# Performance work log

Hardware: AMD Instinct MI355X
Metric: run time of the kernel (lower is better)

Reference implementation:

```python
import math
import jax, jax.numpy as jnp
import numpy as np

B, C, T = 4, 512, 1024
H = 8
KC = C // H
WIN = 4


def _get_relative_embeddings(emb, length):
    win = (emb.shape[1] - 1) // 2
    pad_length = max(length - (win + 1), 0)
    slice_start = max(win + 1 - length, 0)
    slice_end = slice_start + 2 * length - 1
    if pad_length > 0:
        emb = jnp.pad(emb, ((0, 0), (pad_length, pad_length), (0, 0)))
    return emb[:, slice_start:slice_end]


def _relative_to_absolute(x):
    # x: [b, h, L, 2L-1] -> [b, h, L, L] via skew trick
    b, h, L, _ = x.shape
    x = jnp.pad(x, ((0, 0), (0, 0), (0, 0), (0, 1)))          # [b,h,L,2L]
    x_flat = x.reshape(b, h, L * 2 * L)
    x_flat = jnp.pad(x_flat, ((0, 0), (0, 0), (0, L - 1)))    # [b,h,(L+1)(2L-1)]
    x_final = x_flat.reshape(b, h, L + 1, 2 * L - 1)
    return x_final[:, :, :L, L - 1:]


def _absolute_to_relative(x):
    # x: [b, h, L, L] -> [b, h, L, 2L-1]
    b, h, L, _ = x.shape
    x = jnp.pad(x, ((0, 0), (0, 0), (0, 0), (0, L - 1)))      # [b,h,L,2L-1]
    x_flat = x.reshape(b, h, L * (2 * L - 1))
    x_flat = jnp.pad(x_flat, ((0, 0), (0, 0), (L, 0)))        # [b,h,2L^2]
    x_final = x_flat.reshape(b, h, L, 2 * L)
    return x_final[:, :, :, 1:]


def setup_inputs() -> dict:
    key = jax.random.key(0)
    ks = jax.random.split(key, 12)
    xavier = math.sqrt(6.0 / (C + C))  # xavier_uniform for [C, C, 1] conv weight
    rel_std = KC ** (-0.5)
    return {
        "x": jax.random.normal(ks[0], (B, C, T), dtype=jnp.float32),
        "wq": jax.random.uniform(ks[1], (C, C), jnp.float32, -xavier, xavier),
        "bq": jnp.zeros((C,), jnp.float32),
        "wk": jax.random.uniform(ks[2], (C, C), jnp.float32, -xavier, xavier),
        "bk": jnp.zeros((C,), jnp.float32),
        "wv": jax.random.uniform(ks[3], (C, C), jnp.float32, -xavier, xavier),
        "bv": jnp.zeros((C,), jnp.float32),
        "wo": jax.random.normal(ks[4], (C, C), jnp.float32) * (1.0 / math.sqrt(C)),
        "bo": jnp.zeros((C,), jnp.float32),
        "emb_rel_k": jax.random.normal(ks[5], (1, 2 * WIN + 1, KC), jnp.float32) * rel_std,
        "emb_rel_v": jax.random.normal(ks[6], (1, 2 * WIN + 1, KC), jnp.float32) * rel_std,
    }


def reference(x, wq, bq, wk, bk, wv, bv, wo, bo, emb_rel_k, emb_rel_v):
    b, c, t = x.shape
    # 1x1 conv == channel matmul
    q = jnp.einsum("oi,bit->bot", wq, x) + bq[:, None]
    k = jnp.einsum("oi,bit->bot", wk, x) + bk[:, None]
    v = jnp.einsum("oi,bit->bot", wv, x) + bv[:, None]
    # [b, H, t, kc]
    q = q.reshape(b, H, KC, t).transpose(0, 1, 3, 2)
    k = k.reshape(b, H, KC, t).transpose(0, 1, 3, 2)
    v = v.reshape(b, H, KC, t).transpose(0, 1, 3, 2)
    inv_sqrt = 1.0 / math.sqrt(KC)
    scores = jnp.einsum("bhtc,bhsc->bhts", q, k) * inv_sqrt
    rel_k = _get_relative_embeddings(emb_rel_k, t)[0]            # [2t-1, kc]
    rel_logits = jnp.einsum("bhtc,rc->bhtr", q, rel_k)           # [b,h,t,2t-1]
    scores = scores + _relative_to_absolute(rel_logits) * inv_sqrt
    p_attn = jax.nn.softmax(scores, axis=-1)
    output = jnp.einsum("bhts,bhsc->bhtc", p_attn, v)
    rel_weights = _absolute_to_relative(p_attn)                  # [b,h,t,2t-1]
    rel_v = _get_relative_embeddings(emb_rel_v, t)[0]            # [2t-1, kc]
    output = output + jnp.einsum("bhtr,rc->bhtc", rel_weights, rel_v)
    output = output.transpose(0, 1, 3, 2).reshape(b, c, t)
    return jnp.einsum("oi,bit->bot", wo, output) + bo[:, None]
```

## Files before the change

kernel.cpp:

```cpp
#include <hip/hip_runtime.h>
#include <hip/hip_bf16.h>

#define Bdim 4
#define Cdim 512
#define Tdim 1024
#define Hn   8
#define KCd  64

typedef __attribute__((ext_vector_type(8))) short bf16x8;
typedef __attribute__((ext_vector_type(4))) float f32x4;

__device__ __forceinline__ unsigned short f32_bf16_rne(float f) {
    unsigned u = __float_as_uint(f);
    u += 0x7FFFu + ((u >> 16) & 1u);
    return (unsigned short)(u >> 16);
}
__device__ __forceinline__ float bf16_f32(unsigned short h) {
    return __uint_as_float(((unsigned)h) << 16);
}

__device__ __forceinline__ int off_row(int row, int c) {
    return (((row >> 4) * 2 + (c >> 5)) << 9)
         + (((((c >> 3) & 3) << 4) + (row & 15)) << 3) + (c & 7);
}
__device__ __forceinline__ int off_col(int c, int j) {
    return (((c >> 4) * 2 + (j >> 5)) << 9)
         + (((((j >> 3) & 3) << 4) + (c & 15)) << 3) + (j & 7);
}

__device__ __forceinline__ int sw(int row, int col) {
    return (row << 6) + ((((col >> 3) ^ (row & 7)) << 3) | (col & 7));
}
__device__ __forceinline__ bf16x8 fragld(const unsigned short* a, int row, int kstep, int quad) {
    return *(const bf16x8*)&a[(row << 6) + ((((kstep << 2) | quad) ^ (row & 7)) << 3)];
}

#define BM 128
#define BN 64
#define BK 32
#define LDK 40

__global__ __launch_bounds__(256) void gemm3_mfma(
    int mode,
    const float* __restrict__ w0, const float* __restrict__ w1, const float* __restrict__ w2,
    const float* __restrict__ b0, const float* __restrict__ b1, const float* __restrict__ b2,
    const float* __restrict__ x,
    unsigned short* __restrict__ qhi, unsigned short* __restrict__ qlo,
    unsigned short* __restrict__ khi, unsigned short* __restrict__ klo,
    unsigned short* __restrict__ vhi, unsigned short* __restrict__ vlo,
    float* __restrict__ ofp)
{
    __shared__ unsigned short Whi[BM][LDK], Wlo[BM][LDK];
    __shared__ unsigned short Xhi[BN][LDK], Xlo[BN][LDK];

    const int tid = threadIdx.x;

    int bx, by, b;
    {
        const int n = blockIdx.x;
        const int xcd = n & 7, slot = n >> 3;
        if (mode == 0) {
            const int stripe = (xcd << 3) | (slot / 12);
            by = slot % 12;
            bx = stripe & 15;
            b  = stripe >> 4;
        } else {
            const int stripe = (xcd << 3) | (slot >> 2);
            by = slot & 3;
            bx = stripe & 15;
            b  = stripe >> 4;
        }
    }

    const int m_tile = by * BM;
    const int sel = m_tile >> 9;
    const float* W  = sel == 0 ? w0 : (sel == 1 ? w1 : w2);
    const float* Bv = sel == 0 ? b0 : (sel == 1 ? b1 : b2);
    const int m0 = m_tile & 511;
    const int n0 = bx * BN;

    const float* Xb = x + (size_t)b * Cdim * Tdim;

    const int lane = tid & 63, wid = tid >> 6;
    const int wm = (wid & 1) * 64, wn = (wid >> 1) * 32;
    const int l15 = lane & 15, quad = lane >> 4;

    const int wk4 = (tid & 7) * 4;
    const int wmr = tid >> 3;
    const int xn  = tid & 63;
    const int xo  = tid >> 6;

    f32x4 acc[4][2];
    #pragma unroll
    for (int i = 0; i < 4; ++i)
        #pragma unroll
        for (int j = 0; j < 2; ++j) acc[i][j] = (f32x4){0.f, 0.f, 0.f, 0.f};

    for (int k0 = 0; k0 < Cdim; k0 += BK) {
        __syncthreads();

        #pragma unroll
        for (int p = 0; p < 4; ++p) {
            const int m = wmr + p * 32;
            float4 wv = *(const float4*)(W + (size_t)(m0 + m) * Cdim + k0 + wk4);
            ushort4 hi, lo;
            hi.x = f32_bf16_rne(wv.x); lo.x = f32_bf16_rne(wv.x - bf16_f32(hi.x));
            hi.y = f32_bf16_rne(wv.y); lo.y = f32_bf16_rne(wv.y - bf16_f32(hi.y));
            hi.z = f32_bf16_rne(wv.z); lo.z = f32_bf16_rne(wv.z - bf16_f32(hi.z));
            hi.w = f32_bf16_rne(wv.w); lo.w = f32_bf16_rne(wv.w - bf16_f32(hi.w));
            *(ushort4*)&Whi[m][wk4] = hi;
            *(ushort4*)&Wlo[m][wk4] = lo;
        }

        {
            float xv[8];
            #pragma unroll
            for (int kk = 0; kk < 8; ++kk)
                xv[kk] = Xb[(size_t)(k0 + xo * 8 + kk) * Tdim + n0 + xn];
            ushort4 hi0, hi1, lo0, lo1;
            unsigned short h;
            h = f32_bf16_rne(xv[0]); hi0.x = h; lo0.x = f32_bf16_rne(xv[0] - bf16_f32(h));
            h = f32_bf16_rne(xv[1]); hi0.y = h; lo0.y = f32_bf16_rne(xv[1] - bf16_f32(h));
            h = f32_bf16_rne(xv[2]); hi0.z = h; lo0.z = f32_bf16_rne(xv[2] - bf16_f32(h));
            h = f32_bf16_rne(xv[3]); hi0.w = h; lo0.w = f32_bf16_rne(xv[3] - bf16_f32(h));
            h = f32_bf16_rne(xv[4]); hi1.x = h; lo1.x = f32_bf16_rne(xv[4] - bf16_f32(h));
            h = f32_bf16_rne(xv[5]); hi1.y = h; lo1.y = f32_bf16_rne(xv[5] - bf16_f32(h));
            h = f32_bf16_rne(xv[6]); hi1.z = h; lo1.z = f32_bf16_rne(xv[6] - bf16_f32(h));
            h = f32_bf16_rne(xv[7]); hi1.w = h; lo1.w = f32_bf16_rne(xv[7] - bf16_f32(h));
            *(ushort4*)&Xhi[xn][xo * 8]     = hi0;
            *(ushort4*)&Xhi[xn][xo * 8 + 4] = hi1;
            *(ushort4*)&Xlo[xn][xo * 8]     = lo0;
            *(ushort4*)&Xlo[xn][xo * 8 + 4] = lo1;
        }
        __syncthreads();

        bf16x8 ahi[4], alo[4], bhi[2], blo[2];
        #pragma unroll
        for (int mt = 0; mt < 4; ++mt) {
            ahi[mt] = *(const bf16x8*)&Whi[wm + mt * 16 + l15][quad * 8];
            alo[mt] = *(const bf16x8*)&Wlo[wm + mt * 16 + l15][quad * 8];
        }
        #pragma unroll
        for (int nt = 0; nt < 2; ++nt) {
            bhi[nt] = *(const bf16x8*)&Xhi[wn + nt * 16 + l15][quad * 8];
            blo[nt] = *(const bf16x8*)&Xlo[wn + nt * 16 + l15][quad * 8];
        }
        #pragma unroll
        for (int mt = 0; mt < 4; ++mt)
            #pragma unroll
            for (int nt = 0; nt < 2; ++nt) {
                f32x4 c = acc[mt][nt];
                c = __builtin_amdgcn_mfma_f32_16x16x32_bf16(ahi[mt], bhi[nt], c, 0, 0, 0);
                c = __builtin_amdgcn_mfma_f32_16x16x32_bf16(ahi[mt], blo[nt], c, 0, 0, 0);
                c = __builtin_amdgcn_mfma_f32_16x16x32_bf16(alo[mt], bhi[nt], c, 0, 0, 0);
                acc[mt][nt] = c;
            }
    }

    if (mode == 1) {
        float* Ob = ofp + (size_t)b * Cdim * Tdim;
        #pragma unroll
        for (int mt = 0; mt < 4; ++mt) {
            const int mb = m0 + wm + mt * 16 + quad * 4;
            float bb[4];
            #pragma unroll
            for (int r = 0; r < 4; ++r) bb[r] = Bv[mb + r];
            #pragma unroll
            for (int nt = 0; nt < 2; ++nt) {
                const int t = n0 + wn + nt * 16 + l15;
                #pragma unroll
                for (int r = 0; r < 4; ++r)
                    Ob[(size_t)(mb + r) * Tdim + t] = acc[mt][nt][r] + bb[r];
            }
        }
    } else if (sel < 2) {
        unsigned short* phi = sel == 0 ? qhi : khi;
        unsigned short* plo = sel == 0 ? qlo : klo;
        #pragma unroll
        for (int mt = 0; mt < 4; ++mt) {
            const int mv = m0 + wm + mt * 16 + quad * 4;
            const int head = mv >> 6, c0 = mv & 63;
            float bb[4];
            #pragma unroll
            for (int r = 0; r < 4; ++r) bb[r] = Bv[mv + r];
            #pragma unroll
            for (int nt = 0; nt < 2; ++nt) {
                const int t = n0 + wn + nt * 16 + l15;
                const int tile = t >> 6, r_ = t & 63;
                const size_t off = (((size_t)(b * Hn + head) * 16 + tile) << 12)
                                 + (size_t)off_row(r_, c0);
                ushort4 h4, l4;
                float v0 = acc[mt][nt][0] + bb[0];
                float v1 = acc[mt][nt][1] + bb[1];
                float v2 = acc[mt][nt][2] + bb[2];
                float v3 = acc[mt][nt][3] + bb[3];
                h4.x = f32_bf16_rne(v0); l4.x = f32_bf16_rne(v0 - bf16_f32(h4.x));
                h4.y = f32_bf16_rne(v1); l4.y = f32_bf16_rne(v1 - bf16_f32(h4.y));
                h4.z = f32_bf16_rne(v2); l4.z = f32_bf16_rne(v2 - bf16_f32(h4.z));
                h4.w = f32_bf16_rne(v3); l4.w = f32_bf16_rne(v3 - bf16_f32(h4.w));
                *(ushort4*)(phi + off) = h4;
                *(ushort4*)(plo + off) = l4;
            }
        }
    } else {
        #pragma unroll
        for (int mt = 0; mt < 4; ++mt) {
            const int mv = m0 + wm + mt * 16 + quad * 4;
            const int head = mv >> 6;
            float bb[4];
            #pragma unroll
            for (int r = 0; r < 4; ++r) bb[r] = Bv[mv + r];
            #pragma unroll
            for (int nt = 0; nt < 2; ++nt) {
                const int t = n0 + wn + nt * 16 + l15;
                const int tile = t >> 6, jl = t & 63;
                const size_t tb = ((size_t)(b * Hn + head) * 16 + tile) << 12;
                #pragma unroll
                for (int r = 0; r < 4; ++r) {
                    const int cr = (mv & 63) + r;
                    const float v = acc[mt][nt][r] + bb[r];
                    const unsigned short h = f32_bf16_rne(v);
                    const size_t off = tb + off_col(cr, jl);
                    vhi[off] = h;
                    vlo[off] = f32_bf16_rne(v - bf16_f32(h));
                }
            }
        }
    }
}

__global__ __launch_bounds__(256) void attn_mfma(
    const unsigned short* __restrict__ qhi, const unsigned short* __restrict__ qlo,
    const unsigned short* __restrict__ khi, const unsigned short* __restrict__ klo,
    const unsigned short* __restrict__ vhi, const unsigned short* __restrict__ vlo,
    const float* __restrict__ ek,
    const float* __restrict__ ev,
    float* __restrict__ ctx)
{
    __shared__ alignas(16) unsigned short psh[4096], psl[4096];
    __shared__ float rk[576];
    __shared__ float evs[576];

    const int tid = threadIdx.x;

    int it, h, b;
    {
        const int n = blockIdx.x;
        const int xcd = n & 7, slot = n >> 3;
        const int pair = (xcd << 2) | (slot >> 4);
        it = slot & 15;
        b = pair >> 3;
        h = pair & 7;
    }
    const int i0 = it * 64;
    const int lane = tid & 63, w = tid >> 6;
    const int l15 = lane & 15, quad = lane >> 4;
    const int m_blk = w * 16 + l15;
    const int lo8 = lane << 3;

    const size_t bh16 = (size_t)(b * Hn + h) * 16;
    float* ctxb = ctx + ((size_t)b * Cdim + h * KCd) * Tdim;

    bf16x8 qfh[2], qfl[2];
    {
        const unsigned short* qth = qhi + ((bh16 + it) << 12);
        const unsigned short* qtl = qlo + ((bh16 + it) << 12);
        #pragma unroll
        for (int ks = 0; ks < 2; ++ks) {
            qfh[ks] = *(const bf16x8*)(qth + (((w << 1) | ks) << 9) + lo8);
            qfl[ks] = *(const bf16x8*)(qtl + (((w << 1) | ks) << 9) + lo8);
        }
    }

    bf16x8 ekh[2], ekl[2];
    #pragma unroll
    for (int ks = 0; ks < 2; ++ks) {
        #pragma unroll
        for (int j = 0; j < 8; ++j) { ekh[ks][j] = 0; ekl[ks][j] = 0; }
        if (l15 < 9) {
            #pragma unroll
            for (int j = 0; j < 8; ++j) {
                const float v = ek[l15 * 64 + ks * 32 + quad * 8 + j];
                const unsigned short hh = f32_bf16_rne(v);
                ekh[ks][j] = (short)hh;
                ekl[ks][j] = (short)f32_bf16_rne(v - bf16_f32(hh));
            }
        }
    }

    {
        f32x4 rkD = (f32x4){0.f, 0.f, 0.f, 0.f};
        #pragma unroll
        for (int ks = 0; ks < 2; ++ks) {
            rkD = __builtin_amdgcn_mfma_f32_16x16x32_bf16(qfh[ks], ekh[ks], rkD, 0, 0, 0);
            rkD = __builtin_amdgcn_mfma_f32_16x16x32_bf16(qfh[ks], ekl[ks], rkD, 0, 0, 0);
            rkD = __builtin_amdgcn_mfma_f32_16x16x32_bf16(qfl[ks], ekh[ks], rkD, 0, 0, 0);
        }
        if (l15 < 9) {
            #pragma unroll
            for (int r = 0; r < 4; ++r)
                rk[(w * 16 + quad * 4 + r) * 9 + l15] = rkD[r];
        }
    }
    for (int idx = tid; idx < 576; idx += 256) evs[idx] = ev[idx];
    __syncthreads();

    float m_run = -1e30f, l_run = 0.f;
    f32x4 Oc[4];
    #pragma unroll
    for (int ct = 0; ct < 4; ++ct) Oc[ct] = (f32x4){0.f, 0.f, 0.f, 0.f};

    const unsigned short* kh0 = khi + (bh16 << 12);
    const unsigned short* kl0 = klo + (bh16 << 12);
    const unsigned short* vh0 = vhi + (bh16 << 12);
    const unsigned short* vl0 = vlo + (bh16 << 12);

    for (int t = 0; t < 16; ++t) {
        const int j0 = t << 6;
        const size_t tb = (size_t)t << 12;
        const unsigned short* kht = kh0 + tb;
        const unsigned short* klt = kl0 + tb;
        const unsigned short* vht = vh0 + tb;
        const unsigned short* vlt = vl0 + tb;

        bf16x8 vbh[2][4], vbl[2][4];
        #pragma unroll
        for (int ks = 0; ks < 2; ++ks)
            #pragma unroll
            for (int ct = 0; ct < 4; ++ct) {
                vbh[ks][ct] = *(const bf16x8*)(vht + (((ct << 1) | ks) << 9) + lo8);
                vbl[ks][ct] = *(const bf16x8*)(vlt + (((ct << 1) | ks) << 9) + lo8);
            }

        f32x4 Sc[4];
        #pragma unroll
        for (int jt = 0; jt < 4; ++jt) Sc[jt] = (f32x4){0.f, 0.f, 0.f, 0.f};
        #pragma unroll
        for (int ks = 0; ks < 2; ++ks) {
            bf16x8 ah[4], al[4];
            #pragma unroll
            for (int jt = 0; jt < 4; ++jt) {
                ah[jt] = *(const bf16x8*)(kht + (((jt << 1) | ks) << 9) + lo8);
                al[jt] = *(const bf16x8*)(klt + (((jt << 1) | ks) << 9) + lo8);
            }
            #pragma unroll
            for (int jt = 0; jt < 4; ++jt) {
                Sc[jt] = __builtin_amdgcn_mfma_f32_16x16x32_bf16(ah[jt], qfh[ks], Sc[jt], 0, 0, 0);
                Sc[jt] = __builtin_amdgcn_mfma_f32_16x16x32_bf16(ah[jt], qfl[ks], Sc[jt], 0, 0, 0);
                Sc[jt] = __builtin_amdgcn_mfma_f32_16x16x32_bf16(al[jt], qfh[ks], Sc[jt], 0, 0, 0);
            }
        }

        const int dt = j0 - i0;
        const bool diag = (dt >= -67 && dt <= 67);
        if (diag) {
            #pragma unroll
            for (int jt = 0; jt < 4; ++jt) {
                const int db = dt + jt * 16 + quad * 4 - m_blk;
                #pragma unroll
                for (int r = 0; r < 4; ++r) {
                    const int d = db + r;
                    if ((unsigned)(d + 4) <= 8u) Sc[jt][r] += rk[m_blk * 9 + d + 4];
                }
            }
        }

        float mt = -1e30f;
        #pragma unroll
        for (int jt = 0; jt < 4; ++jt)
            #pragma unroll
            for (int r = 0; r < 4; ++r) {
                Sc[jt][r] *= 0.125f;
                mt = fmaxf(mt, Sc[jt][r]);
            }
        mt = fmaxf(mt, __shfl_xor(mt, 16));
        mt = fmaxf(mt, __shfl_xor(mt, 32));
        const float mn = fmaxf(m_run, mt);
        const float alpha = __expf(m_run - mn);
        float rs = 0.f;
        #pragma unroll
        for (int jt = 0; jt < 4; ++jt)
            #pragma unroll
            for (int r = 0; r < 4; ++r) {
                const float e = __expf(Sc[jt][r] - mn);
                Sc[jt][r] = e;
                rs += e;
            }
        rs += __shfl_xor(rs, 16);
        rs += __shfl_xor(rs, 32);
        l_run = l_run * alpha + rs;
        m_run = mn;

        #pragma unroll
        for (int jt = 0; jt < 4; ++jt) {
            ushort4 ph, pl;
            ph.x = f32_bf16_rne(Sc[jt][0]); pl.x = f32_bf16_rne(Sc[jt][0] - bf16_f32(ph.x));
            ph.y = f32_bf16_rne(Sc[jt][1]); pl.y = f32_bf16_rne(Sc[jt][1] - bf16_f32(ph.y));
            ph.z = f32_bf16_rne(Sc[jt][2]); pl.z = f32_bf16_rne(Sc[jt][2] - bf16_f32(ph.z));
            ph.w = f32_bf16_rne(Sc[jt][3]); pl.w = f32_bf16_rne(Sc[jt][3] - bf16_f32(ph.w));
            const int o = sw(m_blk, jt * 16 + quad * 4);
            *(ushort4*)&psh[o] = ph;
            *(ushort4*)&psl[o] = pl;
        }

        const float al0 = __shfl(alpha, quad * 4 + 0);
        const float al1 = __shfl(alpha, quad * 4 + 1);
        const float al2 = __shfl(alpha, quad * 4 + 2);
        const float al3 = __shfl(alpha, quad * 4 + 3);
        #pragma unroll
        for (int ct = 0; ct < 4; ++ct) {
            Oc[ct][0] *= al0; Oc[ct][1] *= al1; Oc[ct][2] *= al2; Oc[ct][3] *= al3;
        }
        #pragma unroll
        for (int ks = 0; ks < 2; ++ks) {
            bf16x8 pah = fragld(psh, m_blk, ks, quad);
            bf16x8 pal = fragld(psl, m_blk, ks, quad);
            #pragma unroll
            for (int ct = 0; ct < 4; ++ct) {
                Oc[ct] = __builtin_amdgcn_mfma_f32_16x16x32_bf16(pah, vbh[ks][ct], Oc[ct], 0, 0, 0);
                Oc[ct] = __builtin_amdgcn_mfma_f32_16x16x32_bf16(pah, vbl[ks][ct], Oc[ct], 0, 0, 0);
                Oc[ct] = __builtin_amdgcn_mfma_f32_16x16x32_bf16(pal, vbh[ks][ct], Oc[ct], 0, 0, 0);
            }
        }

        if (diag) {
            #pragma unroll
            for (int r = 0; r < 4; ++r) {
                const int mrow = w * 16 + quad * 4 + r;
                const int ig = i0 + mrow;
                #pragma unroll
                for (int e = 0; e < 9; ++e) {
                    const int jl = ig + e - 4 - j0;
                    if ((unsigned)jl < 64u) {
                        const int o = sw(mrow, jl);
                        const float p = bf16_f32(psh[o]) + bf16_f32(psl[o]);
                        #pragma unroll
                        for (int ct = 0; ct < 4; ++ct)
                            Oc[ct][r] += p * evs[e * 64 + ct * 16 + l15];
                    }
                }
            }
        }
    }

    const float rlv = 1.f / l_run;
    const float rl0 = __shfl(rlv, quad * 4 + 0);
    const float rl1 = __shfl(rlv, quad * 4 + 1);
    const float rl2 = __shfl(rlv, quad * 4 + 2);
    const float rl3 = __shfl(rlv, quad * 4 + 3);
    #pragma unroll
    for (int ct = 0; ct < 4; ++ct) {
        float4 o4;
        o4.x = Oc[ct][0] * rl0;
        o4.y = Oc[ct][1] * rl1;
        o4.z = Oc[ct][2] * rl2;
        o4.w = Oc[ct][3] * rl3;
        *(float4*)(ctxb + (size_t)(ct * 16 + l15) * Tdim + i0 + w * 16 + quad * 4) = o4;
    }
}

extern "C" void kernel_launch(void* const* d_in, const int* in_sizes, int n_in,
                              void* d_out, int out_size, void* d_ws, size_t ws_size,
                              hipStream_t stream) {
    const float* x  = (const float*)d_in[0];
    const float* wq = (const float*)d_in[1];
    const float* bq = (const float*)d_in[2];
    const float* wk = (const float*)d_in[3];
    const float* bk = (const float*)d_in[4];
    const float* wv = (const float*)d_in[5];
    const float* bv = (const float*)d_in[6];
    const float* wo = (const float*)d_in[7];
    const float* bo = (const float*)d_in[8];
    const float* ek = (const float*)d_in[9];
    const float* ev = (const float*)d_in[10];
    float* out = (float*)d_out;

    const size_t plane = (size_t)Bdim * Cdim * Tdim;
    unsigned short* qhi = (unsigned short*)d_ws;
    unsigned short* qlo = qhi + plane;
    unsigned short* khi = qlo + plane;
    unsigned short* klo = khi + plane;
    unsigned short* vhi = klo + plane;
    unsigned short* vlo = vhi + plane;
    float* cbuf = (float*)(vlo + plane);

    gemm3_mfma<<<dim3(768), 256, 0, stream>>>(
        0, wq, wk, wv, bq, bk, bv, x, qhi, qlo, khi, klo, vhi, vlo, nullptr);

    attn_mfma<<<dim3(512), 256, 0, stream>>>(
        qhi, qlo, khi, klo, vhi, vlo, ek, ev, cbuf);

    gemm3_mfma<<<dim3(256), 256, 0, stream>>>(
        1, wo, wo, wo, bo, bo, bo, cbuf,
        nullptr, nullptr, nullptr, nullptr, nullptr, nullptr, out);
}
```

Measured before the change: 182.8 us.

## Fuse QKV projection, attention and output projection into one persistent kernel

Replaces the three launches (QKV GEMM, attention, output GEMM) with a single persistent kernel of 512 blocks. Phases are separated by software grid barriers built on atomics, and a memset clears the barrier counters before each launch. The aim is to remove launch gaps and tail idle time between kernels. In exchange, the QKV phase now runs 768 tiles over 512 blocks in two passes, which leaves a load imbalance. The launch bounds also cap registers for two blocks per CU, and the barrier deadlocks if not all blocks are co-resident.

Result: slower. 438.4 us (+139.9%).

```diff
diff --git a/kernel.cpp b/kernel.cpp
--- a/kernel.cpp
+++ b/kernel.cpp
@@ -27,7 +27,6 @@
     return (((c >> 4) * 2 + (j >> 5)) << 9)
          + (((((j >> 3) & 3) << 4) + (c & 15)) << 3) + (j & 7);
 }
-
 __device__ __forceinline__ int sw(int row, int col) {
     return (row << 6) + ((((col >> 3) ^ (row & 7)) << 3) | (col & 7));
 }
@@ -35,136 +34,508 @@
     return *(const bf16x8*)&a[(row << 6) + ((((kstep << 2) | quad) ^ (row & 7)) << 3)];
 }
 
-#define BM 128
-#define BN 64
-#define BK 32
-#define LDK 40
-
-__global__ __launch_bounds__(256) void gemm3_mfma(
-    int mode,
-    const float* __restrict__ w0, const float* __restrict__ w1, const float* __restrict__ w2,
-    const float* __restrict__ b0, const float* __restrict__ b1, const float* __restrict__ b2,
+__device__ __forceinline__ void grid_barrier(unsigned* cnt, unsigned* flag, unsigned target) {
+    __syncthreads();
+    if (threadIdx.x == 0) {
+        __threadfence();
+        if (__hip_atomic_fetch_add(cnt, 1u, __ATOMIC_ACQ_REL, __HIP_MEMORY_SCOPE_AGENT) == target - 1u)
+            __hip_atomic_store(flag, 1u, __ATOMIC_RELEASE, __HIP_MEMORY_SCOPE_AGENT);
+        while (__hip_atomic_load(flag, __ATOMIC_ACQUIRE, __HIP_MEMORY_SCOPE_AGENT) == 0u)
+            __builtin_amdgcn_s_sleep(2);
+        __threadfence();
+    }
+    __syncthreads();
+}
+
+__global__ __launch_bounds__(256, 2) void mega_kernel(
     const float* __restrict__ x,
+    const float* __restrict__ wq, const float* __restrict__ bq,
+    const float* __restrict__ wk, const float* __restrict__ bk,
+    const float* __restrict__ wv, const float* __restrict__ bv,
+    const float* __restrict__ wo, const float* __restrict__ bo,
+    const float* __restrict__ ek, const float* __restrict__ ev,
     unsigned short* __restrict__ qhi, unsigned short* __restrict__ qlo,
     unsigned short* __restrict__ khi, unsigned short* __restrict__ klo,
     unsigned short* __restrict__ vhi, unsigned short* __restrict__ vlo,
-    float* __restrict__ ofp)
+    float* __restrict__ cbuf, float* __restrict__ out,
+    unsigned* __restrict__ bar)
 {
-    __shared__ unsigned short Whi[BM][LDK], Wlo[BM][LDK];
-    __shared__ unsigned short Xhi[BN][LDK], Xlo[BN][LDK];
+    __shared__ alignas(16) unsigned char smem[30720];
 
     const int tid = threadIdx.x;
-
-    int bx, by, b;
+    const int bid = blockIdx.x;
+    const int lane = tid & 63, wid = tid >> 6;
+    const int l15 = lane & 15, quad = lane >> 4;
+
     {
-        const int n = blockIdx.x;
-        const int xcd = n & 7, slot = n >> 3;
-        if (mode == 0) {
+        unsigned short* Whi = (unsigned short*)smem;
+        unsigned short* Wlo = Whi + 5120;
+        unsigned short* Xhi = Wlo + 5120;
+        unsigned short* Xlo = Xhi + 2560;
+
+        const int wk4 = (tid & 7) * 4;
+        const int wmr = tid >> 3;
+        const int xn  = tid & 63;
+        const int xo  = tid >> 6;
+        const int wm = (wid & 1) * 64, wn = (wid >> 1) * 32;
+
+        for (int pass = 0; pass < 2; ++pass) {
+            if (pass == 1 && bid >= 256) break;
+            const int job = pass == 0 ? bid : bid + 512;
+            const int xcd = job & 7, slot = job >> 3;
             const int stripe = (xcd << 3) | (slot / 12);
-            by = slot % 12;
-            bx = stripe & 15;
-            b  = stripe >> 4;
-        } else {
-            const int stripe = (xcd << 3) | (slot >> 2);
-            by = slot & 3;
-            bx = stripe & 15;
-            b  = stripe >> 4;
+            const int by = slot % 12;
+            const int bx = stripe & 15;
+            const int b  = stripe >> 4;
+
+            const int m_tile = by * 128;
+            const int sel = m_tile >> 9;
+            const float* W  = sel == 0 ? wq : (sel == 1 ? wk : wv);
+            const float* Bv = sel == 0 ? bq : (sel == 1 ? bk : bv);
+            const int m0 = m_tile & 511;
+            const int n0 = bx * 64;
+            const float* Xb = x + (size_t)b * Cdim * Tdim;
+
+            f32x4 acc[4][2];
+            #pragma unroll
+            for (int i = 0; i < 4; ++i)
+                #pragma unroll
+                for (int j = 0; j < 2; ++j) acc[i][j] = (f32x4){0.f, 0.f, 0.f, 0.f};
+
+            for (int k0 = 0; k0 < Cdim; k0 += 32) {
+                __syncthreads();
+                #pragma unroll
+                for (int p = 0; p < 4; ++p) {
+                    const int m = wmr + p * 32;
+                    float4 wv4 = *(const float4*)(W + (size_t)(m0 + m) * Cdim + k0 + wk4);
+                    ushort4 hi, lo;
+                    hi.x = f32_bf16_rne(wv4.x); lo.x = f32_bf16_rne(wv4.x - bf16_f32(hi.x));
+                    hi.y = f32_bf16_rne(wv4.y); lo.y = f32_bf16_rne(wv4.y - bf16_f32(hi.y));
+                    hi.z = f32_bf16_rne(wv4.z); lo.z = f32_bf16_rne(wv4.z - bf16_f32(hi.z));
+                    hi.w = f32_bf16_rne(wv4.w); lo.w = f32_bf16_rne(wv4.w - bf16_f32(hi.w));
+                    *(ushort4*)&Whi[m * 40 + wk4] = hi;
+                    *(ushort4*)&Wlo[m * 40 + wk4] = lo;
+                }
+                {
+                    float xv[8];
+                    #pragma unroll
+                    for (int kk = 0; kk < 8; ++kk)
+                        xv[kk] = Xb[(size_t)(k0 + xo * 8 + kk) * Tdim + n0 + xn];
+                    ushort4 hi0, hi1, lo0, lo1;
+                    unsigned short h;
+                    h = f32_bf16_rne(xv[0]); hi0.x = h; lo0.x = f32_bf16_rne(xv[0] - bf16_f32(h));
+                    h = f32_bf16_rne(xv[1]); hi0.y = h; lo0.y = f32_bf16_rne(xv[1] - bf16_f32(h));
+                    h = f32_bf16_rne(xv[2]); hi0.z = h; lo0.z = f32_bf16_rne(xv[2] - bf16_f32(h));
+                    h = f32_bf16_rne(xv[3]); hi0.w = h; lo0.w = f32_bf16_rne(xv[3] - bf16_f32(h));
+                    h = f32_bf16_rne(xv[4]); hi1.x = h; lo1.x = f32_bf16_rne(xv[4] - bf16_f32(h));
+                    h = f32_bf16_rne(xv[5]); hi1.y = h; lo1.y = f32_bf16_rne(xv[5] - bf16_f32(h));
+                    h = f32_bf16_rne(xv[6]); hi1.z = h; lo1.z = f32_bf16_rne(xv[6] - bf16_f32(h));
+                    h = f32_bf16_rne(xv[7]); hi1.w = h; lo1.w = f32_bf16_rne(xv[7] - bf16_f32(h));
+                    *(ushort4*)&Xhi[xn * 40 + xo * 8]     = hi0;
+                    *(ushort4*)&Xhi[xn * 40 + xo * 8 + 4] = hi1;
+                    *(ushort4*)&Xlo[xn * 40 + xo * 8]     = lo0;
+                    *(ushort4*)&Xlo[xn * 40 + xo * 8 + 4] = lo1;
+                }
+                __syncthreads();
+
+                bf16x8 ahi[4], alo[4], bhi[2], blo[2];
+                #pragma unroll
+                for (int mt = 0; mt < 4; ++mt) {
+                    ahi[mt] = *(const bf16x8*)&Whi[(wm + mt * 16 + l15) * 40 + quad * 8];
+                    alo[mt] = *(const bf16x8*)&Wlo[(wm + mt * 16 + l15) * 40 + quad * 8];
+                }
+                #pragma unroll
+                for (int nt = 0; nt < 2; ++nt) {
+                    bhi[nt] = *(const bf16x8*)&Xhi[(wn + nt * 16 + l15) * 40 + quad * 8];
+                    blo[nt] = *(const bf16x8*)&Xlo[(wn + nt * 16 + l15) * 40 + quad * 8];
+                }
+                #pragma unroll
+                for (int mt = 0; mt < 4; ++mt)
+                    #pragma unroll
+                    for (int nt = 0; nt < 2; ++nt) {
+                        f32x4 c = acc[mt][nt];
+                        c = __builtin_amdgcn_mfma_f32_16x16x32_bf16(ahi[mt], bhi[nt], c, 0, 0, 0);
+                        c = __builtin_amdgcn_mfma_f32_16x16x32_bf16(ahi[mt], blo[nt], c, 0, 0, 0);
+                        c = __builtin_amdgcn_mfma_f32_16x16x32_bf16(alo[mt], bhi[nt], c, 0, 0, 0);
+                        acc[mt][nt] = c;
+                    }
+            }
+
+            if (sel < 2) {
+                unsigned short* phi = sel == 0 ? qhi : khi;
+                unsigned short* plo = sel == 0 ? qlo : klo;
+                #pragma unroll
+                for (int mt = 0; mt < 4; ++mt) {
+                    const int mv = m0 + wm + mt * 16 + quad * 4;
+                    const int head = mv >> 6, c0 = mv & 63;
+                    float bb[4];
+                    #pragma unroll
+                    for (int r = 0; r < 4; ++r) bb[r] = Bv[mv + r];
+                    #pragma unroll
+                    for (int nt = 0; nt < 2; ++nt) {
+                        const int t = n0 + wn + nt * 16 + l15;
+                        const int tile = t >> 6, r_ = t & 63;
+                        const size_t off = (((size_t)(b * Hn + head) * 16 + tile) << 12)
+                                         + (size_t)off_row(r_, c0);
+                        ushort4 h4, l4;
+                        const float v0 = acc[mt][nt][0] + bb[0];
+                        const float v1 = acc[mt][nt][1] + bb[1];
+                        const float v2 = acc[mt][nt][2] + bb[2];
+                        const float v3 = acc[mt][nt][3] + bb[3];
+                        h4.x = f32_bf16_rne(v0); l4.x = f32_bf16_rne(v0 - bf16_f32(h4.x));
+                        h4.y = f32_bf16_rne(v1); l4.y = f32_bf16_rne(v1 - bf16_f32(h4.y));
+                        h4.z = f32_bf16_rne(v2); l4.z = f32_bf16_rne(v2 - bf16_f32(h4.z));
+                        h4.w = f32_bf16_rne(v3); l4.w = f32_bf16_rne(v3 - bf16_f32(h4.w));
+                        *(ushort4*)(phi + off) = h4;
+                        *(ushort4*)(plo + off) = l4;
+                    }
+                }
+            } else {
+                #pragma unroll
+                for (int mt = 0; mt < 4; ++mt) {
+                    const int mv = m0 + wm + mt * 16 + quad * 4;
+                    const int head = mv >> 6;
+                    float bb[4];
+                    #pragma unroll
+                    for (int r = 0; r < 4; ++r) bb[r] = Bv[mv + r];
+                    #pragma unroll
+                    for (int nt = 0; nt < 2; ++nt) {
+                        const int t = n0 + wn + nt * 16 + l15;
+                        const int tile = t >> 6, jl = t & 63;
+                        const size_t tb = ((size_t)(b * Hn + head) * 16 + tile) << 12;
+                        #pragma unroll
+                        for (int r = 0; r < 4; ++r) {
+                            const int cr = (mv & 63) + r;
+                            const float v = acc[mt][nt][r] + bb[r];
+                            const unsigned short h = f32_bf16_rne(v);
+                            const size_t off = tb + off_col(cr, jl);
+                            vhi[off] = h;
+                            vlo[off] = f32_bf16_rne(v - bf16_f32(h));
+                        }
+                    }
+                }
+            }
         }
     }
 
-    const int m_tile = by * BM;
-    const int sel = m_tile >> 9;
-    const float* W  = sel == 0 ? w0 : (sel == 1 ? w1 : w2);
-    const float* Bv = sel == 0 ? b0 : (sel == 1 ? b1 : b2);
-    const int m0 = m_tile & 511;
-    const int n0 = bx * BN;
-
-    const float* Xb = x + (size_t)b * Cdim * Tdim;
-
-    const int lane = tid & 63, wid = tid >> 6;
-    const int wm = (wid & 1) * 64, wn = (wid >> 1) * 32;
-    const int l15 = lane & 15, quad = lane >> 4;
-
-    const int wk4 = (tid & 7) * 4;
-    const int wmr = tid >> 3;
-    const int xn  = tid & 63;
-    const int xo  = tid >> 6;
-
-    f32x4 acc[4][2];
-    #pragma unroll
-    for (int i = 0; i < 4; ++i)
+    grid_barrier(bar + 0, bar + 1, 512u);
+
+    {
+        unsigned short* psh = (unsigned short*)smem;
+        unsigned short* psl = psh + 4096;
+        float* rk  = (float*)(psl + 4096);
+        float* evs = rk + 576;
+
+        int it, h, b;
+        {
+            const int n = bid;
+            const int xcd = n & 7, slot = n >> 3;
+            const int pair = (xcd << 2) | (slot >> 4);
+            it = slot & 15;
+            b = pair >> 3;
+            h = pair & 7;
+        }
+        const int i0 = it * 64;
+        const int w = wid;
+        const int m_blk = w * 16 + l15;
+        const int lo8 = lane << 3;
+
+        const size_t bh16 = (size_t)(b * Hn + h) * 16;
+        float* ctxb = cbuf + ((size_t)b * Cdim + h * KCd) * Tdim;
+
+        bf16x8 qfh[2], qfl[2];
+        {
+            const unsigned short* qth = qhi + ((bh16 + it) << 12);
+            const unsigned short* qtl = qlo + ((bh16 + it) << 12);
+            #pragma unroll
+            for (int ks = 0; ks < 2; ++ks) {
+                qfh[ks] = *(const bf16x8*)(qth + (((w << 1) | ks) << 9) + lo8);
+                qfl[ks] = *(const bf16x8*)(qtl + (((w << 1) | ks) << 9) + lo8);
+            }
+        }
+
+        bf16x8 ekh[2], ekl[2];
         #pragma unroll
-        for (int j = 0; j < 2; ++j) acc[i][j] = (f32x4){0.f, 0.f, 0.f, 0.f};
-
-    for (int k0 = 0; k0 < Cdim; k0 += BK) {
+        for (int ks = 0; ks < 2; ++ks) {
+            #pragma unroll
+            for (int j = 0; j < 8; ++j) { ekh[ks][j] = 0; ekl[ks][j] = 0; }
+            if (l15 < 9) {
+                #pragma unroll
+                for (int j = 0; j < 8; ++j) {
+                    const float v = ek[l15 * 64 + ks * 32 + quad * 8 + j];
+                    const unsigned short hh = f32_bf16_rne(v);
+                    ekh[ks][j] = (short)hh;
+                    ekl[ks][j] = (short)f32_bf16_rne(v - bf16_f32(hh));
+                }
+            }
+        }
+
+        {
+            f32x4 rkD = (f32x4){0.f, 0.f, 0.f, 0.f};
+            #pragma unroll
+            for (int ks = 0; ks < 2; ++ks) {
+                rkD = __builtin_amdgcn_mfma_f32_16x16x32_bf16(qfh[ks], ekh[ks], rkD, 0, 0, 0);
+                rkD = __builtin_amdgcn_mfma_f32_16x16x32_bf16(qfh[ks], ekl[ks], rkD, 0, 0, 0);
+                rkD = __builtin_amdgcn_mfma_f32_16x16x32_bf16(qfl[ks], ekh[ks], rkD, 0, 0, 0);
+            }
+            if (l15 < 9) {
+                #pragma unroll
+                for (int r = 0; r < 4; ++r)
+                    rk[(w * 16 + quad * 4 + r) * 9 + l15] = rkD[r];
+            }
+        }
+        for (int idx = tid; idx < 576; idx += 256) evs[idx] = ev[idx];
         __syncthreads();
 
+        float m_run = -1e30f, l_run = 0.f;
+        f32x4 Oc[4];
         #pragma unroll
-        for (int p = 0; p < 4; ++p) {
-            const int m = wmr + p * 32;
-            float4 wv = *(const float4*)(W + (size_t)(m0 + m) * Cdim + k0 + wk4);
-            ushort4 hi, lo;
-            hi.x = f32_bf16_rne(wv.x); lo.x = f32_bf16_rne(wv.x - bf16_f32(hi.x));
-            hi.y = f32_bf16_rne(wv.y); lo.y = f32_bf16_rne(wv.y - bf16_f32(hi.y));
-            hi.z = f32_bf16_rne(wv.z); lo.z = f32_bf16_rne(wv.z - bf16_f32(hi.z));
-            hi.w = f32_bf16_rne(wv.w); lo.w = f32_bf16_rne(wv.w - bf16_f32(hi.w));
-            *(ushort4*)&Whi[m][wk4] = hi;
-            *(ushort4*)&Wlo[m][wk4] = lo;
-        }
-
-        {
-            float xv[8];
-            #pragma unroll
-            for (int kk = 0; kk < 8; ++kk)
-                xv[kk] = Xb[(size_t)(k0 + xo * 8 + kk) * Tdim + n0 + xn];
-            ushort4 hi0, hi1, lo0, lo1;
-            unsigned short h;
-            h = f32_bf16_rne(xv[0]); hi0.x = h; lo0.x = f32_bf16_rne(xv[0] - bf16_f32(h));
-            h = f32_bf16_rne(xv[1]); hi0.y = h; lo0.y = f32_bf16_rne(xv[1] - bf16_f32(h));
-            h = f32_bf16_rne(xv[2]); hi0.z = h; lo0.z = f32_bf16_rne(xv[2] - bf16_f32(h));
-            h = f32_bf16_rne(xv[3]); hi0.w = h; lo0.w = f32_bf16_rne(xv[3] - bf16_f32(h));
-            h = f32_bf16_rne(xv[4]); hi1.x = h; lo1.x = f32_bf16_rne(xv[4] - bf16_f32(h));
-            h = f32_bf16_rne(xv[5]); hi1.y = h; lo1.y = f32_bf16_rne(xv[5] - bf16_f32(h));
-            h = f32_bf16_rne(xv[6]); hi1.z = h; lo1.z = f32_bf16_rne(xv[6] - bf16_f32(h));
-            h = f32_bf16_rne(xv[7]); hi1.w = h; lo1.w = f32_bf16_rne(xv[7] - bf16_f32(h));
-            *(ushort4*)&Xhi[xn][xo * 8]     = hi0;
-            *(ushort4*)&Xhi[xn][xo * 8 + 4] = hi1;
-            *(ushort4*)&Xlo[xn][xo * 8]     = lo0;
-            *(ushort4*)&Xlo[xn][xo * 8 + 4] = lo1;
-        }
-        __syncthreads();
-
-        bf16x8 ahi[4], alo[4], bhi[2], blo[2];
+        for (int ct = 0; ct < 4; ++ct) Oc[ct] = (f32x4){0.f, 0.f, 0.f, 0.f};
+
+        const unsigned short* kh0 = khi + (bh16 << 12);
+        const unsigned short* kl0 = klo + (bh16 << 12);
+        const unsigned short* vh0 = vhi + (bh16 << 12);
+        const unsigned short* vl0 = vlo + (bh16 << 12);
+
+        for (int t = 0; t < 16; ++t) {
+            const int j0 = t << 6;
+            const size_t tb = (size_t)t << 12;
+            const unsigned short* kht = kh0 + tb;
+            const unsigned short* klt = kl0 + tb;
+            const unsigned short* vht = vh0 + tb;
+            const unsigned short* vlt = vl0 + tb;
+
+            bf16x8 vbh[2][4], vbl[2][4];
+            #pragma unroll
+            for (int ks = 0; ks < 2; ++ks)
+                #pragma unroll
+                for (int ct = 0; ct < 4; ++ct) {
+                    vbh[ks][ct] = *(const bf16x8*)(vht + (((ct << 1) | ks) << 9) + lo8);
+                    vbl[ks][ct] = *(const bf16x8*)(vlt + (((ct << 1) | ks) << 9) + lo8);
+                }
+
+            f32x4 Sc[4];
+            #pragma unroll
+            for (int jt = 0; jt < 4; ++jt) Sc[jt] = (f32x4){0.f, 0.f, 0.f, 0.f};
+            #pragma unroll
+            for (int ks = 0; ks < 2; ++ks) {
+                bf16x8 ah[4], al[4];
+                #pragma unroll
+                for (int jt = 0; jt < 4; ++jt) {
+                    ah[jt] = *(const bf16x8*)(kht + (((jt << 1) | ks) << 9) + lo8);
+                    al[jt] = *(const bf16x8*)(klt + (((jt << 1) | ks) << 9) + lo8);
+                }
+                #pragma unroll
+                for (int jt = 0; jt < 4; ++jt) {
+                    Sc[jt] = __builtin_amdgcn_mfma_f32_16x16x32_bf16(ah[jt], qfh[ks], Sc[jt], 0, 0, 0);
+                    Sc[jt] = __builtin_amdgcn_mfma_f32_16x16x32_bf16(ah[jt], qfl[ks], Sc[jt], 0, 0, 0);
+                    Sc[jt] = __builtin_amdgcn_mfma_f32_16x16x32_bf16(al[jt], qfh[ks], Sc[jt], 0, 0, 0);
+                }
+            }
+
+            const int dt = j0 - i0;
+            const bool diag = (dt >= -67 && dt <= 67);
+            if (diag) {
+                #pragma unroll
+                for (int jt = 0; jt < 4; ++jt) {
+                    const int db = dt + jt * 16 + quad * 4 - m_blk;
+                    #pragma unroll
+                    for (int r = 0; r < 4; ++r) {
+                        const int d = db + r;
+                        if ((unsigned)(d + 4) <= 8u) Sc[jt][r] += rk[m_blk * 9 + d + 4];
+                    }
+                }
+            }
+
+            float mt = -1e30f;
+            #pragma unroll
+            for (int jt = 0; jt < 4; ++jt)
+                #pragma unroll
+                for (int r = 0; r < 4; ++r) {
+                    Sc[jt][r] *= 0.125f;
+                    mt = fmaxf(mt, Sc[jt][r]);
+                }
+            mt = fmaxf(mt, __shfl_xor(mt, 16));
+            mt = fmaxf(mt, __shfl_xor(mt, 32));
+            const float mn = fmaxf(m_run, mt);
+            const float alpha = __expf(m_run - mn);
+            float rs = 0.f;
+            #pragma unroll
+            for (int jt = 0; jt < 4; ++jt)
+                #pragma unroll
+                for (int r = 0; r < 4; ++r) {
+                    const float e = __expf(Sc[jt][r] - mn);
+                    Sc[jt][r] = e;
+                    rs += e;
+                }
+            rs += __shfl_xor(rs, 16);
+            rs += __shfl_xor(rs, 32);
+            l_run = l_run * alpha + rs;
+            m_run = mn;
+
+            #pragma unroll
+            for (int jt = 0; jt < 4; ++jt) {
+                ushort4 ph, pl;
+                ph.x = f32_bf16_rne(Sc[jt][0]); pl.x = f32_bf16_rne(Sc[jt][0] - bf16_f32(ph.x));
+                ph.y = f32_bf16_rne(Sc[jt][1]); pl.y = f32_bf16_rne(Sc[jt][1] - bf16_f32(ph.y));
+                ph.z = f32_bf16_rne(Sc[jt][2]); pl.z = f32_bf16_rne(Sc[jt][2] - bf16_f32(ph.z));
+                ph.w = f32_bf16_rne(Sc[jt][3]); pl.w = f32_bf16_rne(Sc[jt][3] - bf16_f32(ph.w));
+                const int o = sw(m_blk, jt * 16 + quad * 4);
+                *(ushort4*)&psh[o] = ph;
+                *(ushort4*)&psl[o] = pl;
+            }
+
+            const float al0 = __shfl(alpha, quad * 4 + 0);
+            const float al1 = __shfl(alpha, quad * 4 + 1);
+            const float al2 = __shfl(alpha, quad * 4 + 2);
+            const float al3 = __shfl(alpha, quad * 4 + 3);
+            #pragma unroll
+            for (int ct = 0; ct < 4; ++ct) {
+                Oc[ct][0] *= al0; Oc[ct][1] *= al1; Oc[ct][2] *= al2; Oc[ct][3] *= al3;
+            }
+            #pragma unroll
+            for (int ks = 0; ks < 2; ++ks) {
+                bf16x8 pah = fragld(psh, m_blk, ks, quad);
+                bf16x8 pal = fragld(psl, m_blk, ks, quad);
+                #pragma unroll
+                for (int ct = 0; ct < 4; ++ct) {
+                    Oc[ct] = __builtin_amdgcn_mfma_f32_16x16x32_bf16(pah, vbh[ks][ct], Oc[ct], 0, 0, 0);
+                    Oc[ct] = __builtin_amdgcn_mfma_f32_16x16x32_bf16(pah, vbl[ks][ct], Oc[ct], 0, 0, 0);
+                    Oc[ct] = __builtin_amdgcn_mfma_f32_16x16x32_bf16(pal, vbh[ks][ct], Oc[ct], 0, 0, 0);
+                }
+            }
+
+            if (diag) {
+                #pragma unroll
+                for (int r = 0; r < 4; ++r) {
+                    const int mrow = w * 16 + quad * 4 + r;
+                    const int ig = i0 + mrow;
+                    #pragma unroll
+                    for (int e = 0; e < 9; ++e) {
+                        const int jl = ig + e - 4 - j0;
+                        if ((unsigned)jl < 64u) {
+                            const int o = sw(mrow, jl);
+                            const float p = bf16_f32(psh[o]) + bf16_f32(psl[o]);
+                            #pragma unroll
+                            for (int ct = 0; ct < 4; ++ct)
+                                Oc[ct][r] += p * evs[e * 64 + ct * 16 + l15];
+                        }
+                    }
+                }
+            }
+        }
+
+        const float rlv = 1.f / l_run;
+        const float rl0 = __shfl(rlv, quad * 4 + 0);
+        const float rl1 = __shfl(rlv, quad * 4 + 1);
+        const float rl2 = __shfl(rlv, quad * 4 + 2);
+        const float rl3 = __shfl(rlv, quad * 4 + 3);
         #pragma unroll
-        for (int mt = 0; mt < 4; ++mt) {
-            ahi[mt] = *(const bf16x8*)&Whi[wm + mt * 16 + l15][quad * 8];
-            alo[mt] = *(const bf16x8*)&Wlo[wm + mt * 16 + l15][quad * 8];
-        }
+        for (int ct = 0; ct < 4; ++ct) {
+            float4 o4;
+            o4.x = Oc[ct][0] * rl0;
+            o4.y = Oc[ct][1] * rl1;
+            o4.z = Oc[ct][2] * rl2;
+            o4.w = Oc[ct][3] * rl3;
+            *(float4*)(ctxb + (size_t)(ct * 16 + l15) * Tdim + i0 + w * 16 + quad * 4) = o4;
+        }
+    }
+
+    grid_barrier(bar + 2, bar + 3, 512u);
+
+    if (bid < 256) {
+        unsigned short* Whi = (unsigned short*)smem;
+        unsigned short* Wlo = Whi + 5120;
+        unsigned short* Xhi = Wlo + 5120;
+        unsigned short* Xlo = Xhi + 2560;
+
+        const int wk4 = (tid & 7) * 4;
+        const int wmr = tid >> 3;
+        const int xn  = tid & 63;
+        const int xo  = tid >> 6;
+        const int wm = (wid & 1) * 64, wn = (wid >> 1) * 32;
+
+        const int xcd = bid & 7, slot = bid >> 3;
+        const int stripe = (xcd << 3) | (slot >> 2);
+        const int by = slot & 3;
+        const int bx = stripe & 15;
+        const int b  = stripe >> 4;
+        const int m0 = by * 128;
+        const int n0 = bx * 64;
+        const float* Xb = cbuf + (size_t)b * Cdim * Tdim;
+
+        f32x4 acc[4][2];
         #pragma unroll
-        for (int nt = 0; nt < 2; ++nt) {
-            bhi[nt] = *(const bf16x8*)&Xhi[wn + nt * 16 + l15][quad * 8];
-            blo[nt] = *(const bf16x8*)&Xlo[wn + nt * 16 + l15][quad * 8];
-        }
-        #pragma unroll
-        for (int mt = 0; mt < 4; ++mt)
+        for (int i = 0; i < 4; ++i)
+            #pragma unroll
+            for (int j = 0; j < 2; ++j) acc[i][j] = (f32x4){0.f, 0.f, 0.f, 0.f};
+
+        for (int k0 = 0; k0 < Cdim; k0 += 32) {
+            __syncthreads();
+            #pragma unroll
+            for (int p = 0; p < 4; ++p) {
+                const int m = wmr + p * 32;
+                float4 wv4 = *(const float4*)(wo + (size_t)(m0 + m) * Cdim + k0 + wk4);
+                ushort4 hi, lo;
+                hi.x = f32_bf16_rne(wv4.x); lo.x = f32_bf16_rne(wv4.x - bf16_f32(hi.x));
+                hi.y = f32_bf16_rne(wv4.y); lo.y = f32_bf16_rne(wv4.y - bf16_f32(hi.y));
+                hi.z = f32_bf16_rne(wv4.z); lo.z = f32_bf16_rne(wv4.z - bf16_f32(hi.z));
+                hi.w = f32_bf16_rne(wv4.w); lo.w = f32_bf16_rne(wv4.w - bf16_f32(hi.w));
+                *(ushort4*)&Whi[m * 40 + wk4] = hi;
+                *(ushort4*)&Wlo[m * 40 + wk4] = lo;
+            }
+            {
+                float xv[8];
+                #pragma unroll
+                for (int kk = 0; kk < 8; ++kk)
+                    xv[kk] = Xb[(size_t)(k0 + xo * 8 + kk) * Tdim + n0 + xn];
+                ushort4 hi0, hi1, lo0, lo1;
+                unsigned short h;
+                h = f32_bf16_rne(xv[0]); hi0.x = h; lo0.x = f32_bf16_rne(xv[0] - bf16_f32(h));
+                h = f32_bf16_rne(xv[1]); hi0.y = h; lo0.y = f32_bf16_rne(xv[1] - bf16_f32(h));
+                h = f32_bf16_rne(xv[2]); hi0.z = h; lo0.z = f32_bf16_rne(xv[2] - bf16_f32(h));
+                h = f32_bf16_rne(xv[3]); hi0.w = h; lo0.w = f32_bf16_rne(xv[3] - bf16_f32(h));
+                h = f32_bf16_rne(xv[4]); hi1.x = h; lo1.x = f32_bf16_rne(xv[4] - bf16_f32(h));
+                h = f32_bf16_rne(xv[5]); hi1.y = h; lo1.y = f32_bf16_rne(xv[5] - bf16_f32(h));
+                h = f32_bf16_rne(xv[6]); hi1.z = h; lo1.z = f32_bf16_rne(xv[6] - bf16_f32(h));
+                h = f32_bf16_rne(xv[7]); hi1.w = h; lo1.w = f32_bf16_rne(xv[7] - bf16_f32(h));
+                *(ushort4*)&Xhi[xn * 40 + xo * 8]     = hi0;
+                *(ushort4*)&Xhi[xn * 40 + xo * 8 + 4] = hi1;
+                *(ushort4*)&Xlo[xn * 40 + xo * 8]     = lo0;
+                *(ushort4*)&Xlo[xn * 40 + xo * 8 + 4] = lo1;
+            }
+            __syncthreads();
+
+            bf16x8 ahi[4], alo[4], bhi[2], blo[2];
+            #pragma unroll
+            for (int mt = 0; mt < 4; ++mt) {
+                ahi[mt] = *(const bf16x8*)&Whi[(wm + mt * 16 + l15) * 40 + quad * 8];
+                alo[mt] = *(const bf16x8*)&Wlo[(wm + mt * 16 + l15) * 40 + quad * 8];
+            }
             #pragma unroll
             for (int nt = 0; nt < 2; ++nt) {
-                f32x4 c = acc[mt][nt];
-                c = __builtin_amdgcn_mfma_f32_16x16x32_bf16(ahi[mt], bhi[nt], c, 0, 0, 0);
-                c = __builtin_amdgcn_mfma_f32_16x16x32_bf16(ahi[mt], blo[nt], c, 0, 0, 0);
-                c = __builtin_amdgcn_mfma_f32_16x16x32_bf16(alo[mt], bhi[nt], c, 0, 0, 0);
-                acc[mt][nt] = c;
-            }
-    }
-
-    if (mode == 1) {
-        float* Ob = ofp + (size_t)b * Cdim * Tdim;
+                bhi[nt] = *(const bf16x8*)&Xhi[(wn + nt * 16 + l15) * 40 + quad * 8];
+                blo[nt] = *(const bf16x8*)&Xlo[(wn + nt * 16 + l15) * 40 + quad * 8];
+            }
+            #pragma unroll
+            for (int mt = 0; mt < 4; ++mt)
+                #pragma unroll
+                for (int nt = 0; nt < 2; ++nt) {
+                    f32x4 c = acc[mt][nt];
+                    c = __builtin_amdgcn_mfma_f32_16x16x32_bf16(ahi[mt], bhi[nt], c, 0, 0, 0);
+                    c = __builtin_amdgcn_mfma_f32_16x16x32_bf16(ahi[mt], blo[nt], c, 0, 0, 0);
+                    c = __builtin_amdgcn_mfma_f32_16x16x32_bf16(alo[mt], bhi[nt], c, 0, 0, 0);
+                    acc[mt][nt] = c;
+                }
+        }
+
+        float* Ob = out + (size_t)b * Cdim * Tdim;
         #pragma unroll
         for (int mt = 0; mt < 4; ++mt) {
             const int mb = m0 + wm + mt * 16 + quad * 4;
             float bb[4];
             #pragma unroll
-            for (int r = 0; r < 4; ++r) bb[r] = Bv[mb + r];
+            for (int r = 0; r < 4; ++r) bb[r] = bo[mb + r];
             #pragma unroll
             for (int nt = 0; nt < 2; ++nt) {
                 const int t = n0 + wn + nt * 16 + l15;
@@ -173,289 +544,6 @@
                     Ob[(size_t)(mb + r) * Tdim + t] = acc[mt][nt][r] + bb[r];
             }
         }
-    } else if (sel < 2) {
-        unsigned short* phi = sel == 0 ? qhi : khi;
-        unsigned short* plo = sel == 0 ? qlo : klo;
-        #pragma unroll
-        for (int mt = 0; mt < 4; ++mt) {
-            const int mv = m0 + wm + mt * 16 + quad * 4;
-            const int head = mv >> 6, c0 = mv & 63;
-            float bb[4];
-            #pragma unroll
-            for (int r = 0; r < 4; ++r) bb[r] = Bv[mv + r];
-            #pragma unroll
-            for (int nt = 0; nt < 2; ++nt) {
-                const int t = n0 + wn + nt * 16 + l15;
-                const int tile = t >> 6, r_ = t & 63;
-                const size_t off = (((size_t)(b * Hn + head) * 16 + tile) << 12)
-                                 + (size_t)off_row(r_, c0);
-                ushort4 h4, l4;
-                float v0 = acc[mt][nt][0] + bb[0];
-                float v1 = acc[mt][nt][1] + bb[1];
-                float v2 = acc[mt][nt][2] + bb[2];
-                float v3 = acc[mt][nt][3] + bb[3];
-                h4.x = f32_bf16_rne(v0); l4.x = f32_bf16_rne(v0 - bf16_f32(h4.x));
-                h4.y = f32_bf16_rne(v1); l4.y = f32_bf16_rne(v1 - bf16_f32(h4.y));
-                h4.z = f32_bf16_rne(v2); l4.z = f32_bf16_rne(v2 - bf16_f32(h4.z));
-                h4.w = f32_bf16_rne(v3); l4.w = f32_bf16_rne(v3 - bf16_f32(h4.w));
-                *(ushort4*)(phi + off) = h4;
-                *(ushort4*)(plo + off) = l4;
-            }
-        }
-    } else {
-        #pragma unroll
-        for (int mt = 0; mt < 4; ++mt) {
-            const int mv = m0 + wm + mt * 16 + quad * 4;
-            const int head = mv >> 6;
-            float bb[4];
-            #pragma unroll
-            for (int r = 0; r < 4; ++r) bb[r] = Bv[mv + r];
-            #pragma unroll
-            for (int nt = 0; nt < 2; ++nt) {
-                const int t = n0 + wn + nt * 16 + l15;
-                const int tile = t >> 6, jl = t & 63;
-                const size_t tb = ((size_t)(b * Hn + head) * 16 + tile) << 12;
-                #pragma unroll
-                for (int r = 0; r < 4; ++r) {
-                    const int cr = (mv & 63) + r;
-                    const float v = acc[mt][nt][r] + bb[r];
-                    const unsigned short h = f32_bf16_rne(v);
-                    const size_t off = tb + off_col(cr, jl);
-                    vhi[off] = h;
-                    vlo[off] = f32_bf16_rne(v - bf16_f32(h));
-                }
-            }
-        }
-    }
-}
-
-__global__ __launch_bounds__(256) void attn_mfma(
-    const unsigned short* __restrict__ qhi, const unsigned short* __restrict__ qlo,
-    const unsigned short* __restrict__ khi, const unsigned short* __restrict__ klo,
-    const unsigned short* __restrict__ vhi, const unsigned short* __restrict__ vlo,
-    const float* __restrict__ ek,
-    const float* __restrict__ ev,
-    float* __restrict__ ctx)
-{
-    __shared__ alignas(16) unsigned short psh[4096], psl[4096];
-    __shared__ float rk[576];
-    __shared__ float evs[576];
-
-    const int tid = threadIdx.x;
-
-    int it, h, b;
-    {
-        const int n = blockIdx.x;
-        const int xcd = n & 7, slot = n >> 3;
-        const int pair = (xcd << 2) | (slot >> 4);
-        it = slot & 15;
-        b = pair >> 3;
-        h = pair & 7;
-    }
-    const int i0 = it * 64;
-    const int lane = tid & 63, w = tid >> 6;
-    const int l15 = lane & 15, quad = lane >> 4;
-    const int m_blk = w * 16 + l15;
-    const int lo8 = lane << 3;
-
-    const size_t bh16 = (size_t)(b * Hn + h) * 16;
-    float* ctxb = ctx + ((size_t)b * Cdim + h * KCd) * Tdim;
-
-    bf16x8 qfh[2], qfl[2];
-    {
-        const unsigned short* qth = qhi + ((bh16 + it) << 12);
-        const unsigned short* qtl = qlo + ((bh16 + it) << 12);
-        #pragma unroll
-        for (int ks = 0; ks < 2; ++ks) {
-            qfh[ks] = *(const bf16x8*)(qth + (((w << 1) | ks) << 9) + lo8);
-            qfl[ks] = *(const bf16x8*)(qtl + (((w << 1) | ks) << 9) + lo8);
-        }
-    }
-
-    bf16x8 ekh[2], ekl[2];
-    #pragma unroll
-    for (int ks = 0; ks < 2; ++ks) {
-        #pragma unroll
-        for (int j = 0; j < 8; ++j) { ekh[ks][j] = 0; ekl[ks][j] = 0; }
-        if (l15 < 9) {
-            #pragma unroll
-            for (int j = 0; j < 8; ++j) {
-                const float v = ek[l15 * 64 + ks * 32 + quad * 8 + j];
-                const unsigned short hh = f32_bf16_rne(v);
-                ekh[ks][j] = (short)hh;
-                ekl[ks][j] = (short)f32_bf16_rne(v - bf16_f32(hh));
-            }
-        }
-    }
-
-    {
-        f32x4 rkD = (f32x4){0.f, 0.f, 0.f, 0.f};
-        #pragma unroll
-        for (int ks = 0; ks < 2; ++ks) {
-            rkD = __builtin_amdgcn_mfma_f32_16x16x32_bf16(qfh[ks], ekh[ks], rkD, 0, 0, 0);
-            rkD = __builtin_amdgcn_mfma_f32_16x16x32_bf16(qfh[ks], ekl[ks], rkD, 0, 0, 0);
-            rkD = __builtin_amdgcn_mfma_f32_16x16x32_bf16(qfl[ks], ekh[ks], rkD, 0, 0, 0);
-        }
-        if (l15 < 9) {
-            #pragma unroll
-            for (int r = 0; r < 4; ++r)
-                rk[(w * 16 + quad * 4 + r) * 9 + l15] = rkD[r];
-        }
-    }
-    for (int idx = tid; idx < 576; idx += 256) evs[idx] = ev[idx];
-    __syncthreads();
-
-    float m_run = -1e30f, l_run = 0.f;
-    f32x4 Oc[4];
-    #pragma unroll
-    for (int ct = 0; ct < 4; ++ct) Oc[ct] = (f32x4){0.f, 0.f, 0.f, 0.f};
-
-    const unsigned short* kh0 = khi + (bh16 << 12);
-    const unsigned short* kl0 = klo + (bh16 << 12);
-    const unsigned short* vh0 = vhi + (bh16 << 12);
-    const unsigned short* vl0 = vlo + (bh16 << 12);
-
-    for (int t = 0; t < 16; ++t) {
-        const int j0 = t << 6;
-        const size_t tb = (size_t)t << 12;
-        const unsigned short* kht = kh0 + tb;
-        const unsigned short* klt = kl0 + tb;
-        const unsigned short* vht = vh0 + tb;
-        const unsigned short* vlt = vl0 + tb;
-
-        bf16x8 vbh[2][4], vbl[2][4];
-        #pragma unroll
-        for (int ks = 0; ks < 2; ++ks)
-            #pragma unroll
-            for (int ct = 0; ct < 4; ++ct) {
-                vbh[ks][ct] = *(const bf16x8*)(vht + (((ct << 1) | ks) << 9) + lo8);
-                vbl[ks][ct] = *(const bf16x8*)(vlt + (((ct << 1) | ks) << 9) + lo8);
-            }
-
-        f32x4 Sc[4];
-        #pragma unroll
-        for (int jt = 0; jt < 4; ++jt) Sc[jt] = (f32x4){0.f, 0.f, 0.f, 0.f};
-        #pragma unroll
-        for (int ks = 0; ks < 2; ++ks) {
-            bf16x8 ah[4], al[4];
-            #pragma unroll
-            for (int jt = 0; jt < 4; ++jt) {
-                ah[jt] = *(const bf16x8*)(kht + (((jt << 1) | ks) << 9) + lo8);
-                al[jt] = *(const bf16x8*)(klt + (((jt << 1) | ks) << 9) + lo8);
-            }
-            #pragma unroll
-            for (int jt = 0; jt < 4; ++jt) {
-                Sc[jt] = __builtin_amdgcn_mfma_f32_16x16x32_bf16(ah[jt], qfh[ks], Sc[jt], 0, 0, 0);
-                Sc[jt] = __builtin_amdgcn_mfma_f32_16x16x32_bf16(ah[jt], qfl[ks], Sc[jt], 0, 0, 0);
-                Sc[jt] = __builtin_amdgcn_mfma_f32_16x16x32_bf16(al[jt], qfh[ks], Sc[jt], 0, 0, 0);
-            }
-        }
-
-        const int dt = j0 - i0;
-        const bool diag = (dt >= -67 && dt <= 67);
-        if (diag) {
-            #pragma unroll
-            for (int jt = 0; jt < 4; ++jt) {
-                const int db = dt + jt * 16 + quad * 4 - m_blk;
-                #pragma unroll
-                for (int r = 0; r < 4; ++r) {
-                    const int d = db + r;
-                    if ((unsigned)(d + 4) <= 8u) Sc[jt][r] += rk[m_blk * 9 + d + 4];
-                }
-            }
-        }
-
-        float mt = -1e30f;
-        #pragma unroll
-        for (int jt = 0; jt < 4; ++jt)
-            #pragma unroll
-            for (int r = 0; r < 4; ++r) {
-                Sc[jt][r] *= 0.125f;
-                mt = fmaxf(mt, Sc[jt][r]);
-            }
-        mt = fmaxf(mt, __shfl_xor(mt, 16));
-        mt = fmaxf(mt, __shfl_xor(mt, 32));
-        const float mn = fmaxf(m_run, mt);
-        const float alpha = __expf(m_run - mn);
-        float rs = 0.f;
-        #pragma unroll
-        for (int jt = 0; jt < 4; ++jt)
-            #pragma unroll
-            for (int r = 0; r < 4; ++r) {
-                const float e = __expf(Sc[jt][r] - mn);
-                Sc[jt][r] = e;
-                rs += e;
-            }
-        rs += __shfl_xor(rs, 16);
-        rs += __shfl_xor(rs, 32);
-        l_run = l_run * alpha + rs;
-        m_run = mn;
-
-        #pragma unroll
-        for (int jt = 0; jt < 4; ++jt) {
-            ushort4 ph, pl;
-            ph.x = f32_bf16_rne(Sc[jt][0]); pl.x = f32_bf16_rne(Sc[jt][0] - bf16_f32(ph.x));
-            ph.y = f32_bf16_rne(Sc[jt][1]); pl.y = f32_bf16_rne(Sc[jt][1] - bf16_f32(ph.y));
-            ph.z = f32_bf16_rne(Sc[jt][2]); pl.z = f32_bf16_rne(Sc[jt][2] - bf16_f32(ph.z));
-            ph.w = f32_bf16_rne(Sc[jt][3]); pl.w = f32_bf16_rne(Sc[jt][3] - bf16_f32(ph.w));
-            const int o = sw(m_blk, jt * 16 + quad * 4);
-            *(ushort4*)&psh[o] = ph;
-            *(ushort4*)&psl[o] = pl;
-        }
-
-        const float al0 = __shfl(alpha, quad * 4 + 0);
-        const float al1 = __shfl(alpha, quad * 4 + 1);
-        const float al2 = __shfl(alpha, quad * 4 + 2);
-        const float al3 = __shfl(alpha, quad * 4 + 3);
-        #pragma unroll
-        for (int ct = 0; ct < 4; ++ct) {
-            Oc[ct][0] *= al0; Oc[ct][1] *= al1; Oc[ct][2] *= al2; Oc[ct][3] *= al3;
-        }
-        #pragma unroll
-        for (int ks = 0; ks < 2; ++ks) {
-            bf16x8 pah = fragld(psh, m_blk, ks, quad);
-            bf16x8 pal = fragld(psl, m_blk, ks, quad);
-            #pragma unroll
-            for (int ct = 0; ct < 4; ++ct) {
-                Oc[ct] = __builtin_amdgcn_mfma_f32_16x16x32_bf16(pah, vbh[ks][ct], Oc[ct], 0, 0, 0);
-                Oc[ct] = __builtin_amdgcn_mfma_f32_16x16x32_bf16(pah, vbl[ks][ct], Oc[ct], 0, 0, 0);
-                Oc[ct] = __builtin_amdgcn_mfma_f32_16x16x32_bf16(pal, vbh[ks][ct], Oc[ct], 0, 0, 0);
-            }
-        }
-
-        if (diag) {
-            #pragma unroll
-            for (int r = 0; r < 4; ++r) {
-                const int mrow = w * 16 + quad * 4 + r;
-                const int ig = i0 + mrow;
-                #pragma unroll
-                for (int e = 0; e < 9; ++e) {
-                    const int jl = ig + e - 4 - j0;
-                    if ((unsigned)jl < 64u) {
-                        const int o = sw(mrow, jl);
-                        const float p = bf16_f32(psh[o]) + bf16_f32(psl[o]);
-                        #pragma unroll
-                        for (int ct = 0; ct < 4; ++ct)
-                            Oc[ct][r] += p * evs[e * 64 + ct * 16 + l15];
-                    }
-                }
-            }
-        }
-    }
-
-    const float rlv = 1.f / l_run;
-    const float rl0 = __shfl(rlv, quad * 4 + 0);
-    const float rl1 = __shfl(rlv, quad * 4 + 1);
-    const float rl2 = __shfl(rlv, quad * 4 + 2);
-    const float rl3 = __shfl(rlv, quad * 4 + 3);
-    #pragma unroll
-    for (int ct = 0; ct < 4; ++ct) {
-        float4 o4;
-        o4.x = Oc[ct][0] * rl0;
-        o4.y = Oc[ct][1] * rl1;
-        o4.z = Oc[ct][2] * rl2;
-        o4.w = Oc[ct][3] * rl3;
-        *(float4*)(ctxb + (size_t)(ct * 16 + l15) * Tdim + i0 + w * 16 + quad * 4) = o4;
     }
 }
 
@@ -483,14 +571,11 @@
     unsigned short* vhi = klo + plane;
     unsigned short* vlo = vhi + plane;
     float* cbuf = (float*)(vlo + plane);
-
-    gemm3_mfma<<<dim3(768), 256, 0, stream>>>(
-        0, wq, wk, wv, bq, bk, bv, x, qhi, qlo, khi, klo, vhi, vlo, nullptr);
-
-    attn_mfma<<<dim3(512), 256, 0, stream>>>(
-        qhi, qlo, khi, klo, vhi, vlo, ek, ev, cbuf);
-
-    gemm3_mfma<<<dim3(256), 256, 0, stream>>>(
-        1, wo, wo, wo, bo, bo, bo, cbuf,
-        nullptr, nullptr, nullptr, nullptr, nullptr, nullptr, out);
-}
+    unsigned* bar = (unsigned*)(cbuf + plane);
+
+    hipMemsetAsync(bar, 0, 64, stream);
+
+    mega_kernel<<<dim3(512), 256, 0, stream>>>(
+        x, wq, bq, wk, bk, wv, bv, wo, bo, ek, ev,
+        qhi, qlo, khi, klo, vhi, vlo, cbuf, out, bar);
+}
```
